# Performance work log

Measured on AMD Instinct MI355X. Metric: run time of the kernel, lower is better.

Reference implementation:

```python
import math
import jax, jax.numpy as jnp
import numpy as np

B, T, C, H = 2, 2048, 1024, 16
HD = C // H
ALPHA = 32.0


def setup_inputs() -> dict:
    key = jax.random.key(0)
    ks = jax.random.split(key, 16)
    s = 0.02
    inp = {
        "query": jax.random.normal(ks[0], (B, T, C), jnp.float32),
        "key": jax.random.normal(ks[1], (B, T, C), jnp.float32),
        "value": jax.random.normal(ks[2], (B, T, C), jnp.float32),
        # causal mask: 0 => masked (matches masked_fill(att_mask == 0, -inf))
        "att_mask": jnp.tril(jnp.ones((1, 1, T, T), jnp.float32)),
        "Wq": jax.random.normal(ks[3], (C, C), jnp.float32) * s,
        "bq": jnp.zeros((C,), jnp.float32),
        "Wk": jax.random.normal(ks[4], (C, C), jnp.float32) * s,
        "bk": jnp.zeros((C,), jnp.float32),
        "Wv": jax.random.normal(ks[5], (C, C), jnp.float32) * s,
        "bv": jnp.zeros((C,), jnp.float32),
        "Wp": jax.random.normal(ks[6], (C, C), jnp.float32) * s,
        "bp": jnp.zeros((C,), jnp.float32),
    }
    return inp


def reference(query, key, value, att_mask, Wq, bq, Wk, bk, Wv, bv, Wp, bp):
    b, tq, c = query.shape
    tk = key.shape[1]
    # separate QKV projections, split heads: [B,H,T,HD]
    q = (query @ Wq + bq).reshape(b, tq, H, HD).transpose(0, 2, 1, 3)
    k = (key @ Wk + bk).reshape(b, tk, H, HD).transpose(0, 2, 1, 3)
    v = (value @ Wv + bv).reshape(b, tk, H, HD).transpose(0, 2, 1, 3)
    # PBrelax: pre-scale q by 1/(alpha*sqrt(hd)), subtract detached global abs-max, rescale
    att = jnp.einsum("bhqd,bhkd->bhqk", q * (1.0 / ALPHA / math.sqrt(HD)), k)
    att = (att - jax.lax.stop_gradient(jnp.max(jnp.abs(att)))) * ALPHA
    att = jnp.where(att_mask[:, :, :tq, :tk] == 0, -jnp.inf, att)
    att = jax.nn.softmax(att, axis=-1)
    y = jnp.einsum("bhqk,bhkd->bhqd", att, v)
    y = y.transpose(0, 2, 1, 3).reshape(b, tq, c)
    return y @ Wp + bp
```

## Files before the change

### kernel.cpp

```cpp
#include <hip/hip_runtime.h>


#define Bsz 2
#define Tsz 2048
#define Csz 1024
#define Hsz 16
#define HDsz 64

typedef __bf16 bf16;
typedef __bf16 bf16x8 __attribute__((ext_vector_type(8)));
typedef float float4v __attribute__((ext_vector_type(4)));

#define MFMA16(a, b, c) __builtin_amdgcn_mfma_f32_16x16x32_bf16(a, b, c, 0, 0, 0)

#define GLOAD_LDS16(gptr, lptr)                                      \
  __builtin_amdgcn_global_load_lds(                                  \
      (const __attribute__((address_space(1))) void*)(gptr),         \
      (__attribute__((address_space(3))) void*)(lptr), 16, 0, 0)

__global__ __launch_bounds__(256) void cast3_bf16(
    const float* __restrict__ q, const float* __restrict__ k,
    const float* __restrict__ v, bf16* __restrict__ oq,
    bf16* __restrict__ ok, bf16* __restrict__ ov) {
  const int z = blockIdx.z;
  const float* src = z == 0 ? q : (z == 1 ? k : v);
  bf16* dst = z == 0 ? oq : (z == 1 ? ok : ov);
  const size_t i = ((size_t)blockIdx.x * 256 + threadIdx.x) * 8;
  const float4 a = *(const float4*)(src + i);
  const float4 b = *(const float4*)(src + i + 4);
  bf16x8 o;
  o[0] = (bf16)a.x; o[1] = (bf16)a.y; o[2] = (bf16)a.z; o[3] = (bf16)a.w;
  o[4] = (bf16)b.x; o[5] = (bf16)b.y; o[6] = (bf16)b.z; o[7] = (bf16)b.w;
  *(bf16x8*)(dst + i) = o;
}

__global__ __launch_bounds__(256) void wtrans_bf16(
    const float* __restrict__ Wq, const float* __restrict__ Wk,
    const float* __restrict__ Wv, const float* __restrict__ Wp,
    bf16* __restrict__ WT) {
  const int z = blockIdx.z;
  const float* W = z == 0 ? Wq : (z == 1 ? Wk : (z == 2 ? Wv : Wp));
  bf16* out = WT + (size_t)z * (Csz * Csz);
  __shared__ float Ts[64][68];
  const int k0 = blockIdx.y * 64, n0 = blockIdx.x * 64;
  const int tid = threadIdx.x;
#pragma unroll
  for (int it = 0; it < 4; ++it) {
    const int idx = it * 256 + tid;
    const int r = idx >> 4, c4 = (idx & 15) * 4;
    *(float4*)&Ts[r][c4] = *(const float4*)(W + (size_t)(k0 + r) * Csz + n0 + c4);
  }
  __syncthreads();
#pragma unroll
  for (int it = 0; it < 2; ++it) {
    const int idx = it * 256 + tid;
    const int n = idx & 63, k8 = (idx >> 6) * 8;
    bf16x8 o;
#pragma unroll
    for (int j = 0; j < 8; ++j) o[j] = (bf16)Ts[k8 + j][n];
    *(bf16x8*)(out + (size_t)(n0 + n) * Csz + k0 + k8) = o;
  }
}

template <typename OutT, bool VTR>
__global__ __launch_bounds__(256) void gemm_mfma(
    const bf16* __restrict__ A0, const bf16* __restrict__ A1,
    const bf16* __restrict__ A2, const bf16* __restrict__ Wt,
    const float* __restrict__ b0, const float* __restrict__ b1,
    const float* __restrict__ b2, OutT* __restrict__ C0,
    OutT* __restrict__ C1, OutT* __restrict__ C2, int M, int N, int K) {
  const int z = blockIdx.z;
  const bf16* A = z == 0 ? A0 : (z == 1 ? A1 : A2);
  const float* bias = z == 0 ? b0 : (z == 1 ? b1 : b2);
  OutT* C = z == 0 ? C0 : (z == 1 ? C1 : C2);
  const bf16* Bt = Wt + (size_t)z * N * K;
  const float osc = (VTR && z == 0) ? 0.180336880111124f : 1.0f;

  __shared__ bf16 As[128 * 32];
  __shared__ bf16 Bs[128 * 32];
  const int tid = threadIdx.x;
  const int wave = tid >> 6, lane = tid & 63;
  const int l15 = lane & 15, quad = lane >> 4;
  const int m0 = blockIdx.y * 128, n0 = blockIdx.x * 128;
  const int wm = (wave >> 1) * 64, wn = (wave & 1) * 64;
  const int srow = tid >> 2, schunk = tid & 3;

  float4v acc[4][4];
#pragma unroll
  for (int i = 0; i < 4; ++i)
#pragma unroll
    for (int j = 0; j < 4; ++j) acc[i][j] = (float4v){0.f, 0.f, 0.f, 0.f};

  for (int k0 = 0; k0 < K; k0 += 32) {
    __syncthreads();
#pragma unroll
    for (int p = 0; p < 2; ++p) {
      const int row = p * 64 + srow;
      GLOAD_LDS16(A + (size_t)(m0 + row) * K + k0 + schunk * 8,
                  &As[(p * 256 + tid) * 8]);
      GLOAD_LDS16(Bt + (size_t)(n0 + row) * K + k0 + schunk * 8,
                  &Bs[(p * 256 + tid) * 8]);
    }
    __syncthreads();

    bf16x8 af[4], bfr[4];
#pragma unroll
    for (int i = 0; i < 4; ++i)
      af[i] = *(const bf16x8*)&As[(wm + i * 16 + l15) * 32 + quad * 8];
#pragma unroll
    for (int j = 0; j < 4; ++j)
      bfr[j] = *(const bf16x8*)&Bs[(wn + j * 16 + l15) * 32 + quad * 8];
#pragma unroll
    for (int i = 0; i < 4; ++i)
#pragma unroll
      for (int j = 0; j < 4; ++j)
        acc[i][j] = MFMA16(af[i], bfr[j], acc[i][j]);
  }

  const int omb = m0 + wm + quad * 4;
  const int onb = n0 + wn + l15;
  if (VTR && z == 2) {
#pragma unroll
    for (int j = 0; j < 4; ++j) {
      const int n = onb + j * 16;
      const float bj = bias[n];
#pragma unroll
      for (int i = 0; i < 4; ++i) {
        const int mrow = omb + i * 16;
        const int bb = mrow >> 11, t = mrow & (Tsz - 1);
        union { bf16 h[4]; uint2 u; } pk;
#pragma unroll
        for (int r = 0; r < 4; ++r) pk.h[r] = (bf16)(acc[i][j][r] + bj);
        *(uint2*)((bf16*)C + ((size_t)(bb * 1024 + n)) * Tsz + t) = pk.u;
      }
    }
  } else {
#pragma unroll
    for (int j = 0; j < 4; ++j) {
      const float bj = bias[onb + j * 16];
#pragma unroll
      for (int i = 0; i < 4; ++i) {
#pragma unroll
        for (int r = 0; r < 4; ++r) {
          const float v = (acc[i][j][r] + bj) * osc;
          const size_t off = (size_t)(omb + i * 16 + r) * N + onb + j * 16;
          if constexpr (sizeof(OutT) == 2)
            C[off] = (OutT)v;
          else
            C[off] = v;
        }
      }
    }
  }
}

__global__ __launch_bounds__(256) void attn_mfma(const bf16* __restrict__ Q,
                                                 const bf16* __restrict__ K,
                                                 const bf16* __restrict__ Vt,
                                                 bf16* __restrict__ Y) {
  __shared__ bf16 Ks[2][64 * 64];
  __shared__ bf16 Vs[2][64 * 64];
  __shared__ bf16 Ps[4][1024];

  const int bh = blockIdx.y;
  const int b = bh >> 4, h = bh & 15;
  const int i0 = (int)(gridDim.x - 1 - blockIdx.x) * 64;
  const int tid = threadIdx.x;
  const int wave = tid >> 6, lane = tid & 63;
  const int l15 = lane & 15, quad = lane >> 4;

  const int srow = tid >> 3;
  const int sch = tid & 7;

  bf16x8 qf0, qf1;
  {
    const bf16* qp =
        Q + ((size_t)(b * Tsz + i0 + wave * 16 + l15)) * Csz + h * HDsz + quad * 8;
    qf0 = *(const bf16x8*)qp;
    qf1 = *(const bf16x8*)(qp + 32);
  }

  bf16x8 ones;
#pragma unroll
  for (int j = 0; j < 8; ++j) ones[j] = (bf16)1.0f;

  float4v Of[4];
  float4v accl = (float4v){0.f, 0.f, 0.f, 0.f};
#pragma unroll
  for (int nc = 0; nc < 4; ++nc) Of[nc] = (float4v){0.f, 0.f, 0.f, 0.f};

  const int qg = i0 + wave * 16 + quad * 4;
  const int ntile = i0 / 64 + 1;

  const bf16* kb = K + (size_t)b * Tsz * Csz + h * HDsz;
  const bf16* vb = Vt + (size_t)bh * HDsz * Tsz;

#pragma unroll
  for (int p = 0; p < 2; ++p) {
    const int r = p * 32 + srow;
    const int c = sch ^ (r & 7);
    GLOAD_LDS16(kb + (size_t)r * Csz + c * 8, &Ks[0][(p * 256 + tid) * 8]);
    GLOAD_LDS16(vb + (size_t)r * Tsz + c * 8, &Vs[0][(p * 256 + tid) * 8]);
  }

  for (int t = 0; t < ntile; ++t) {
    const int j0 = t * 64;
    const int buf = t & 1;
    __syncthreads();
    if (t + 1 < ntile) {
#pragma unroll
      for (int p = 0; p < 2; ++p) {
        const int r = p * 32 + srow;
        const int c = sch ^ (r & 7);
        GLOAD_LDS16(kb + (size_t)(j0 + 64 + r) * Csz + c * 8,
                    &Ks[buf ^ 1][(p * 256 + tid) * 8]);
        GLOAD_LDS16(vb + (size_t)r * Tsz + (j0 + 64) + c * 8,
                    &Vs[buf ^ 1][(p * 256 + tid) * 8]);
      }
    }

    float4v S[4];
#pragma unroll
    for (int nc = 0; nc < 4; ++nc) {
      const int row = nc * 16 + l15;
      const bf16x8 k0 =
          *(const bf16x8*)&Ks[buf][row * 64 + ((quad ^ (row & 7)) * 8)];
      const bf16x8 k1 =
          *(const bf16x8*)&Ks[buf][row * 64 + (((quad + 4) ^ (row & 7)) * 8)];
      float4v a = (float4v){0.f, 0.f, 0.f, 0.f};
      a = MFMA16(qf0, k0, a);
      a = MFMA16(qf1, k1, a);
      S[nc] = a;
    }

    if (j0 + 63 > i0 + wave * 16) {
#pragma unroll
      for (int nc = 0; nc < 4; ++nc)
#pragma unroll
        for (int r = 0; r < 4; ++r)
          if (j0 + nc * 16 + l15 > qg + r) S[nc][r] = -1e30f;
    }

#pragma unroll
    for (int nc = 0; nc < 4; ++nc) {
      const int keyl = nc * 16 + l15;
      const int kc = keyl >> 5;
      const int jj = keyl & 7;
      const int Lhi = ((keyl >> 3) & 3) * 16;
#pragma unroll
      for (int r = 0; r < 4; ++r) {
        const float p = __builtin_amdgcn_exp2f(S[nc][r]);
        Ps[wave][kc * 512 + (Lhi + quad * 4 + r) * 8 + jj] = (bf16)p;
      }
    }

    const bf16x8 pf0 = *(const bf16x8*)&Ps[wave][0 * 512 + lane * 8];
    const bf16x8 pf1 = *(const bf16x8*)&Ps[wave][1 * 512 + lane * 8];
    accl = MFMA16(pf0, ones, accl);
    accl = MFMA16(pf1, ones, accl);
#pragma unroll
    for (int nc = 0; nc < 4; ++nc) {
      const int row = nc * 16 + l15;
      const bf16x8 v0 =
          *(const bf16x8*)&Vs[buf][row * 64 + ((quad ^ (row & 7)) * 8)];
      const bf16x8 v1 =
          *(const bf16x8*)&Vs[buf][row * 64 + (((quad + 4) ^ (row & 7)) * 8)];
      Of[nc] = MFMA16(pf0, v0, Of[nc]);
      Of[nc] = MFMA16(pf1, v1, Of[nc]);
    }
  }

  float rl[4];
#pragma unroll
  for (int r = 0; r < 4; ++r) rl[r] = __builtin_amdgcn_rcpf(accl[r]);
#pragma unroll
  for (int nc = 0; nc < 4; ++nc) {
#pragma unroll
    for (int r = 0; r < 4; ++r) {
      const size_t row = (size_t)b * Tsz + i0 + wave * 16 + quad * 4 + r;
      Y[row * Csz + h * HDsz + nc * 16 + l15] = (bf16)(Of[nc][r] * rl[r]);
    }
  }
}

extern "C" void kernel_launch(void* const* d_in, const int* in_sizes, int n_in,
                              void* d_out, int out_size, void* d_ws,
                              size_t ws_size, hipStream_t stream) {
  const float* query = (const float*)d_in[0];
  const float* key = (const float*)d_in[1];
  const float* value = (const float*)d_in[2];
  const float* Wq = (const float*)d_in[4];
  const float* bq = (const float*)d_in[5];
  const float* Wk = (const float*)d_in[6];
  const float* bk = (const float*)d_in[7];
  const float* Wv = (const float*)d_in[8];
  const float* bv = (const float*)d_in[9];
  const float* Wp = (const float*)d_in[10];
  const float* bp = (const float*)d_in[11];
  float* out = (float*)d_out;

  char* ws = (char*)d_ws;
  bf16* WT = (bf16*)(ws);
  bf16* vc = (bf16*)(ws + (8u << 20));
  bf16* Qp = (bf16*)(ws + (16u << 20));
  bf16* Kp = (bf16*)(ws + (24u << 20));
  bf16* Vt = (bf16*)(ws + (32u << 20));
  bf16* Yb = vc;
  bf16* qc = (bf16*)d_out;
  bf16* kc = (bf16*)((char*)d_out + (8u << 20));

  const int M = Bsz * Tsz;

  cast3_bf16<<<dim3((M * Csz) / (256 * 8), 1, 3), dim3(256), 0, stream>>>(
      query, key, value, qc, kc, vc);
  wtrans_bf16<<<dim3(16, 16, 4), dim3(256), 0, stream>>>(Wq, Wk, Wv, Wp, WT);
  gemm_mfma<bf16, true><<<dim3(Csz / 128, M / 128, 3), dim3(256), 0, stream>>>(
      qc, kc, vc, WT, bq, bk, bv, Qp, Kp, Vt, M, Csz, Csz);
  attn_mfma<<<dim3(Tsz / 64, Bsz * Hsz), dim3(256), 0, stream>>>(Qp, Kp, Vt,
                                                                 Yb);
  gemm_mfma<float, false><<<dim3(Csz / 128, M / 128, 1), dim3(256), 0, stream>>>(
      Yb, Yb, Yb, WT + 3u * (Csz * Csz), bp, bp, bp, out, out, out, M, Csz,
      Csz);
}
```

Measured before the change: 276.0 us.

## Double query rows per attention block and transpose MFMA operands for reuse

Each attention block now handles 128 query rows, with every wave owning two 16-row subtiles. Each K and V fragment loaded from LDS is therefore reused across two MFMAs, and K/V tiles are shared by twice as many queries. The MFMA operand order is swapped so that S and O come out transposed. P can then be written to a padded LDS buffer as vector stores, and outputs go out as 8-byte packed stores. The trade-off is half as many blocks (512 instead of 1024), which lowers parallelism, plus higher register use and extra work on the partially masked causal tiles.

```diff
diff --git a/kernel.cpp b/kernel.cpp
--- a/kernel.cpp
+++ b/kernel.cpp
@@ -9,6 +9,7 @@
 
 typedef __bf16 bf16;
 typedef __bf16 bf16x8 __attribute__((ext_vector_type(8)));
+typedef __bf16 bf16x4 __attribute__((ext_vector_type(4)));
 typedef float float4v __attribute__((ext_vector_type(4)));
 
 #define MFMA16(a, b, c) __builtin_amdgcn_mfma_f32_16x16x32_bf16(a, b, c, 0, 0, 0)
@@ -160,11 +161,11 @@
                                                  bf16* __restrict__ Y) {
   __shared__ bf16 Ks[2][64 * 64];
   __shared__ bf16 Vs[2][64 * 64];
-  __shared__ bf16 Ps[4][1024];
+  __shared__ bf16 Ps[4][32 * 72];
 
   const int bh = blockIdx.y;
   const int b = bh >> 4, h = bh & 15;
-  const int i0 = (int)(gridDim.x - 1 - blockIdx.x) * 64;
+  const int i0 = (int)(gridDim.x - 1 - blockIdx.x) * 128;
   const int tid = threadIdx.x;
   const int wave = tid >> 6, lane = tid & 63;
   const int l15 = lane & 15, quad = lane >> 4;
@@ -172,28 +173,34 @@
   const int srow = tid >> 3;
   const int sch = tid & 7;
 
-  bf16x8 qf0, qf1;
-  {
-    const bf16* qp =
-        Q + ((size_t)(b * Tsz + i0 + wave * 16 + l15)) * Csz + h * HDsz + quad * 8;
-    qf0 = *(const bf16x8*)qp;
-    qf1 = *(const bf16x8*)(qp + 32);
-  }
-
-  bf16x8 ones;
-#pragma unroll
-  for (int j = 0; j < 8; ++j) ones[j] = (bf16)1.0f;
-
-  float4v Of[4];
-  float4v accl = (float4v){0.f, 0.f, 0.f, 0.f};
-#pragma unroll
-  for (int nc = 0; nc < 4; ++nc) Of[nc] = (float4v){0.f, 0.f, 0.f, 0.f};
-
-  const int qg = i0 + wave * 16 + quad * 4;
-  const int ntile = i0 / 64 + 1;
-
   const bf16* kb = K + (size_t)b * Tsz * Csz + h * HDsz;
   const bf16* vb = Vt + (size_t)bh * HDsz * Tsz;
+
+  const int qb = i0 + wave * 32;
+
+  bf16x8 qf[2][2];
+#pragma unroll
+  for (int sub = 0; sub < 2; ++sub) {
+    const bf16* qp =
+        Q + ((size_t)(b * Tsz + qb + sub * 16 + l15)) * Csz + h * HDsz + quad * 8;
+    qf[sub][0] = *(const bf16x8*)qp;
+    qf[sub][1] = *(const bf16x8*)(qp + 32);
+  }
+
+  bf16x8 ones;
+#pragma unroll
+  for (int j = 0; j < 8; ++j) ones[j] = (bf16)1.0f;
+
+  float4v Of[2][4];
+  float4v accl[2];
+#pragma unroll
+  for (int sub = 0; sub < 2; ++sub) {
+    accl[sub] = (float4v){0.f, 0.f, 0.f, 0.f};
+#pragma unroll
+    for (int nc = 0; nc < 4; ++nc) Of[sub][nc] = (float4v){0.f, 0.f, 0.f, 0.f};
+  }
+
+  const int ntile = i0 / 64 + 2;
 
 #pragma unroll
   for (int p = 0; p < 2; ++p) {
@@ -219,66 +226,86 @@
       }
     }
 
-    float4v S[4];
+    if (j0 <= qb + 31) {
+      float4v S[2][4];
+#pragma unroll
+      for (int nc = 0; nc < 4; ++nc) {
+        const int row = nc * 16 + l15;
+        const bf16x8 k0 =
+            *(const bf16x8*)&Ks[buf][row * 64 + ((quad ^ (row & 7)) * 8)];
+        const bf16x8 k1 =
+            *(const bf16x8*)&Ks[buf][row * 64 + (((quad + 4) ^ (row & 7)) * 8)];
+#pragma unroll
+        for (int sub = 0; sub < 2; ++sub) {
+          float4v a = (float4v){0.f, 0.f, 0.f, 0.f};
+          a = MFMA16(k0, qf[sub][0], a);
+          a = MFMA16(k1, qf[sub][1], a);
+          S[sub][nc] = a;
+        }
+      }
+
+      if (j0 + 63 > qb) {
+#pragma unroll
+        for (int sub = 0; sub < 2; ++sub) {
+          const int q = qb + sub * 16 + l15;
+#pragma unroll
+          for (int nc = 0; nc < 4; ++nc) {
+            const int keyb = j0 + nc * 16 + quad * 4;
+#pragma unroll
+            for (int r = 0; r < 4; ++r)
+              if (keyb + r > q) S[sub][nc][r] = -1e30f;
+          }
+        }
+      }
+
+#pragma unroll
+      for (int sub = 0; sub < 2; ++sub) {
+#pragma unroll
+        for (int nc = 0; nc < 4; ++nc) {
+          bf16x4 pk;
+#pragma unroll
+          for (int r = 0; r < 4; ++r)
+            pk[r] = (bf16)__builtin_amdgcn_exp2f(S[sub][nc][r]);
+          *(bf16x4*)&Ps[wave][(sub * 16 + l15) * 72 + nc * 16 + quad * 4] = pk;
+        }
+      }
+
+      bf16x8 pf[2][2];
+#pragma unroll
+      for (int sub = 0; sub < 2; ++sub) {
+#pragma unroll
+        for (int kc = 0; kc < 2; ++kc)
+          pf[sub][kc] = *(const bf16x8*)
+              &Ps[wave][(sub * 16 + l15) * 72 + kc * 32 + quad * 8];
+        accl[sub] = MFMA16(ones, pf[sub][0], accl[sub]);
+        accl[sub] = MFMA16(ones, pf[sub][1], accl[sub]);
+      }
+#pragma unroll
+      for (int nc = 0; nc < 4; ++nc) {
+        const int row = nc * 16 + l15;
+#pragma unroll
+        for (int kc = 0; kc < 2; ++kc) {
+          const bf16x8 vf = *(const bf16x8*)
+              &Vs[buf][row * 64 + (((kc * 4 + quad) ^ (row & 7)) * 8)];
+#pragma unroll
+          for (int sub = 0; sub < 2; ++sub)
+            Of[sub][nc] = MFMA16(vf, pf[sub][kc], Of[sub][nc]);
+        }
+      }
+    }
+  }
+
+#pragma unroll
+  for (int sub = 0; sub < 2; ++sub) {
+    const float rl = __builtin_amdgcn_rcpf(accl[sub][0]);
+    const size_t rowoff =
+        ((size_t)(b * Tsz + qb + sub * 16 + l15)) * Csz + h * HDsz;
 #pragma unroll
     for (int nc = 0; nc < 4; ++nc) {
-      const int row = nc * 16 + l15;
-      const bf16x8 k0 =
-          *(const bf16x8*)&Ks[buf][row * 64 + ((quad ^ (row & 7)) * 8)];
-      const bf16x8 k1 =
-          *(const bf16x8*)&Ks[buf][row * 64 + (((quad + 4) ^ (row & 7)) * 8)];
-      float4v a = (float4v){0.f, 0.f, 0.f, 0.f};
-      a = MFMA16(qf0, k0, a);
-      a = MFMA16(qf1, k1, a);
-      S[nc] = a;
-    }
-
-    if (j0 + 63 > i0 + wave * 16) {
-#pragma unroll
-      for (int nc = 0; nc < 4; ++nc)
-#pragma unroll
-        for (int r = 0; r < 4; ++r)
-          if (j0 + nc * 16 + l15 > qg + r) S[nc][r] = -1e30f;
-    }
-
-#pragma unroll
-    for (int nc = 0; nc < 4; ++nc) {
-      const int keyl = nc * 16 + l15;
-      const int kc = keyl >> 5;
-      const int jj = keyl & 7;
-      const int Lhi = ((keyl >> 3) & 3) * 16;
-#pragma unroll
-      for (int r = 0; r < 4; ++r) {
-        const float p = __builtin_amdgcn_exp2f(S[nc][r]);
-        Ps[wave][kc * 512 + (Lhi + quad * 4 + r) * 8 + jj] = (bf16)p;
-      }
-    }
-
-    const bf16x8 pf0 = *(const bf16x8*)&Ps[wave][0 * 512 + lane * 8];
-    const bf16x8 pf1 = *(const bf16x8*)&Ps[wave][1 * 512 + lane * 8];
-    accl = MFMA16(pf0, ones, accl);
-    accl = MFMA16(pf1, ones, accl);
-#pragma unroll
-    for (int nc = 0; nc < 4; ++nc) {
-      const int row = nc * 16 + l15;
-      const bf16x8 v0 =
-          *(const bf16x8*)&Vs[buf][row * 64 + ((quad ^ (row & 7)) * 8)];
-      const bf16x8 v1 =
-          *(const bf16x8*)&Vs[buf][row * 64 + (((quad + 4) ^ (row & 7)) * 8)];
-      Of[nc] = MFMA16(pf0, v0, Of[nc]);
-      Of[nc] = MFMA16(pf1, v1, Of[nc]);
-    }
-  }
-
-  float rl[4];
-#pragma unroll
-  for (int r = 0; r < 4; ++r) rl[r] = __builtin_amdgcn_rcpf(accl[r]);
-#pragma unroll
-  for (int nc = 0; nc < 4; ++nc) {
-#pragma unroll
-    for (int r = 0; r < 4; ++r) {
-      const size_t row = (size_t)b * Tsz + i0 + wave * 16 + quad * 4 + r;
-      Y[row * Csz + h * HDsz + nc * 16 + l15] = (bf16)(Of[nc][r] * rl[r]);
+      union { bf16 h4[4]; uint2 u; } pk;
+#pragma unroll
+      for (int r = 0; r < 4; ++r) pk.h4[r] = (bf16)(Of[sub][nc][r] * rl);
+      *(uint2*)(Y + rowoff + nc * 16 + quad * 4) = pk.u;
     }
   }
 }
@@ -316,8 +343,8 @@
   wtrans_bf16<<<dim3(16, 16, 4), dim3(256), 0, stream>>>(Wq, Wk, Wv, Wp, WT);
   gemm_mfma<bf16, true><<<dim3(Csz / 128, M / 128, 3), dim3(256), 0, stream>>>(
       qc, kc, vc, WT, bq, bk, bv, Qp, Kp, Vt, M, Csz, Csz);
-  attn_mfma<<<dim3(Tsz / 64, Bsz * Hsz), dim3(256), 0, stream>>>(Qp, Kp, Vt,
-                                                                 Yb);
+  attn_mfma<<<dim3(Tsz / 128, Bsz * Hsz), dim3(256), 0, stream>>>(Qp, Kp, Vt,
+                                                                  Yb);
   gemm_mfma<float, false><<<dim3(Csz / 128, M / 128, 1), dim3(256), 0, stream>>>(
       Yb, Yb, Yb, WT + 3u * (Csz * Csz), bp, bp, bp, out, out, out, M, Csz,
       Csz);
```

After: 271.5 us. About the same (-1.6%).
